# Optimization experiments

Measured on AMD Instinct MI355X. Metric: run time of the kernel, lower is better.

Reference implementation:

```python
import jax, jax.numpy as jnp
import numpy as np

W_WIN, ETA, NSUB, GAP = 5, 0.5, 2, 1e-6

# ---------------- host-side (detached) partition helpers ----------------

def _softmax_np(x):
    e = np.exp(x - x.max())
    return e / e.sum()

def _jsd_np(p, q):
    p = p + 1e-8; p = p / p.sum()
    q = q + 1e-8; q = q / q.sum()
    m = 0.5 * (p + q)
    return float(0.5 * (p * np.log(p / m)).sum() + 0.5 * (q * np.log(q / m)).sum())

def _make_increasing_np(t, gap=GAP):
    t = t.copy()
    for i in range(1, len(t)):
        if t[i] - t[i - 1] < gap:
            t[i] = t[i - 1] + gap
    return t

def _apt_partition(embs, times, w=W_WIN, eta=ETA):
    n = len(times)
    if n < 2 * w:
        return [times[0], times[-1]], [(0, n - 1)]
    bounds = [times[0]]; starts = [0]; j = 0
    while j <= n - 2 * w:
        pl = _softmax_np(embs[j:j + w].mean(0))
        pr = _softmax_np(embs[j + w:j + 2 * w].mean(0))
        if _jsd_np(pl, pr) > eta:
            bounds.append((times[j + w - 1] + times[j + w]) / 2.0)
            starts.append(j + w)
            j += w
        else:
            j += 1
    if times[-1] > bounds[-1]:
        bounds.append(times[-1])
    segs = []
    for i, s in enumerate(starts):
        e = starts[i + 1] - 1 if i + 1 < len(starts) else n - 1
        segs.append((s, e))
    return bounds, segs

def _build_plans(enc_np, ht_np, hl_np, pt_np):
    # mirrors encoded.detach() + .item()/.tolist() in the torch code: the
    # change-point partition and time grids are concrete / non-differentiable
    plans = []
    for b in range(enc_np.shape[0]):
        Lb = int(hl_np[b])
        times = [float(t) for t in ht_np[b, :Lb]]
        bounds, segs = _apt_partition(enc_np[b, :Lb], times)
        seg_plans = []
        for si, (s, e) in enumerate(segs):
            t0 = bounds[si]
            t1 = bounds[si + 1] if si + 1 < len(bounds) else bounds[-1]
            ats = sorted(set([t0, t1] + [t for t in times[s:e + 1] if t0 <= t <= t1]))
            ts = _make_increasing_np(np.asarray(ats, np.float64))
            sel = [int(np.argmin(np.abs(ts - ti))) for ti in times[s:e + 1]]
            seg_plans.append((s, e, (ts[1:] - ts[:-1]).astype(np.float32), sel))
        tail = None
        if float(pt_np[b]) > bounds[-1] + 1e-6:
            s, e = segs[-1]
            ts = _make_increasing_np(np.asarray([bounds[-1], float(pt_np[b])], np.float64))
            tail = (s, e, (ts[1:] - ts[:-1]).astype(np.float32))
        plans.append((seg_plans, tail))
    return plans

# ---------------- differentiable forward ----------------

def _forward(params, plans, u, hi, pos, neg):
    (emb_table, mlp_w1, mlp_b1, mlp_w2, mlp_b2, user_table,
     vf_w1, vf_b1, vf_w2, vf_b2, vf_w3, vf_b3) = params
    B, L = hi.shape
    # Encoder: mlp(emb(ids))
    encoded = jax.nn.relu(emb_table[hi] @ mlp_w1 + mlp_b1) @ mlp_w2 + mlp_b2  # (B,L,d)

    def vf(z, env):  # augmented state [z, env]; env part has zero derivative
        x = jnp.concatenate([z, env])
        h1 = jax.nn.softplus(x @ vf_w1 + vf_b1)
        h2 = jax.nn.softplus(h1 @ vf_w2 + vf_b2)
        return h2 @ vf_w3 + vf_b3

    def integrate(z0, env, dts):  # fixed-step Euler, NSUB substeps per interval
        def step(z, dt):
            for _ in range(NSUB):
                z = z + (dt / NSUB) * vf(z, env)
            return z, z
        _, traj = jax.lax.scan(step, z0, jnp.asarray(dts))
        return jnp.concatenate([z0[None], traj], 0)  # (K, d)

    z_out, tz_out = [], []
    for b in range(B):
        seg_plans, tail = plans[b]
        z = user_table[u[b]]
        tz = []
        for (s, e, dts, sel) in seg_plans:
            env = encoded[b, s:e + 1].mean(0)
            if len(dts) == 0:  # degenerate segment (unreachable with this data)
                tz.extend([z] * (e - s + 1))
                continue
            zt = integrate(z, env, dts)
            tz.extend([zt[i] for i in sel])  # state-at-nearest-grid-time matching
            z = zt[-1]
        if tail is not None:  # evolve up to prediction time t_target
            s, e, dts = tail
            z = integrate(z, encoded[b, s:e + 1].mean(0), dts)[-1]
        z_out.append(z)
        tz_out.append(jnp.stack(tz))
    z_final = jnp.stack(z_out)          # (B,d)
    traj_z = jnp.stack(tz_out)          # (B,L,d) evolved states at interaction times
    traj_t = encoded                    # traj targets = encoded items in order
    s_pos = jnp.sum(z_final * emb_table[pos], -1)
    s_neg = jnp.sum(z_final * emb_table[neg], -1)
    return jnp.concatenate([s_pos[:, None], s_neg[:, None],
                            traj_z.reshape(B, -1), traj_t.reshape(B, -1)], -1)


def setup_inputs():
    key = jax.random.key(0)
    ks = jax.random.split(key, 16)
    n_users, n_items, d, h = 10000, 200000, 128, 512
    B, L = 4, 128
    def xavier(k, shape):
        s = (2.0 / (shape[0] + shape[1])) ** 0.5
        return (jax.random.normal(k, shape) * s).astype(jnp.float32)
    inp = {
        'emb_table': xavier(ks[0], (n_items, d)).at[0].set(0.0),  # padding_idx=0
        'mlp_w1': xavier(ks[1], (d, d)), 'mlp_b1': jnp.zeros((d,), jnp.float32),
        'mlp_w2': xavier(ks[2], (d, d)), 'mlp_b2': jnp.zeros((d,), jnp.float32),
        'user_table': xavier(ks[3], (n_users, d)),
        'vf_w1': xavier(ks[4], (2 * d, h)), 'vf_b1': jnp.zeros((h,), jnp.float32),
        'vf_w2': xavier(ks[5], (h, h)), 'vf_b2': jnp.zeros((h,), jnp.float32),
        'vf_w3': xavier(ks[6], (h, d)), 'vf_b3': jnp.zeros((d,), jnp.float32),
        'u': jax.random.randint(ks[7], (B,), 0, n_users),
        'hi': jax.random.randint(ks[8], (B, L), 1, n_items),
        'ht': jnp.sort(jax.random.uniform(ks[9], (B, L)) * 10.0, axis=1).astype(jnp.float32),
        'hl': jnp.full((B,), L, dtype=jnp.int32),
        'pos': jax.random.randint(ks[10], (B,), 1, n_items),
        'neg': jax.random.randint(ks[11], (B,), 1, n_items),
    }
    inp['pt'] = inp['ht'][:, -1] + 1.0
    return inp


def reference(emb_table, mlp_w1, mlp_b1, mlp_w2, mlp_b2, user_table,
              vf_w1, vf_b1, vf_w2, vf_b2, vf_w3, vf_b3,
              u, hi, ht, hl, pt, pos, neg):
    params = (emb_table, mlp_w1, mlp_b1, mlp_w2, mlp_b2, user_table,
              vf_w1, vf_b1, vf_w2, vf_b2, vf_w3, vf_b3)
    enc_np = np.asarray(jax.nn.relu(emb_table[hi] @ mlp_w1 + mlp_b1) @ mlp_w2 + mlp_b2)
    plans = _build_plans(enc_np, np.asarray(ht), np.asarray(hl), np.asarray(pt))
    return _forward(params, plans, u, hi, pos, neg)
```

## Files before the change

### kernel.cpp

```cpp
#include <hip/hip_runtime.h>
#include <math.h>

#define W_WIN 5
#define NSUB 2
#define MAX_SEG 64
#define MAX_T 256
#define NWGB 8
#define CALIB_END 6

__device__ __forceinline__ float softplusf(float v) {
    return fmaxf(v, 0.0f) + log1pf(expf(-fabsf(v)));
}

__device__ __forceinline__ float npsum128(float e0, float e1) {
    int lane = threadIdx.x & 63;
    int k = lane & 7;
    float r = __shfl(e0, k, 64);
    #pragma unroll
    for (int m = 1; m < 8; ++m) r += __shfl(e0, k + 8 * m, 64);
    #pragma unroll
    for (int m = 0; m < 8; ++m) r += __shfl(e1, k + 8 * m, 64);
    float r0 = __shfl(r, 0, 64), r1 = __shfl(r, 1, 64), r2 = __shfl(r, 2, 64), r3 = __shfl(r, 3, 64);
    float r4 = __shfl(r, 4, 64), r5 = __shfl(r, 5, 64), r6 = __shfl(r, 6, 64), r7 = __shfl(r, 7, 64);
    return ((r0 + r1) + (r2 + r3)) + ((r4 + r5) + (r6 + r7));
}

__device__ __forceinline__ float wmax128(float e0, float e1) {
    float m = fmaxf(e0, e1);
    #pragma unroll
    for (int s = 1; s < 64; s <<= 1) m = fmaxf(m, __shfl_xor(m, s, 64));
    return m;
}

__global__ void encode_kernel(const float* __restrict__ emb, const int* __restrict__ hi,
                              const float* __restrict__ w1, const float* __restrict__ b1,
                              const float* __restrict__ w2, const float* __restrict__ b2,
                              float* __restrict__ enc, float* __restrict__ out,
                              int B, int L, int D) {
    __shared__ float x[128];
    __shared__ float h[128];
    int row = blockIdx.x;
    int j = threadIdx.x;
    int idx = hi[row];
    x[j] = emb[(size_t)idx * D + j];
    __syncthreads();
    float s = b1[j];
    #pragma unroll 8
    for (int i = 0; i < 128; ++i) s += x[i] * w1[i * 128 + j];
    h[j] = fmaxf(s, 0.0f);
    __syncthreads();
    float o = b2[j];
    #pragma unroll 8
    for (int i = 0; i < 128; ++i) o += h[i] * w2[i * 128 + j];
    enc[(size_t)row * D + j] = o;
    int b = row / L, l = row % L;
    size_t OS = 2 + 2 * (size_t)L * D;
    out[(size_t)b * OS + 2 + (size_t)L * D + (size_t)l * D + j] = o;
}

__global__ __launch_bounds__(64) void jsd_kernel(
        const float* __restrict__ enc_all, const int* __restrict__ hl,
        float* __restrict__ jsdv, int L, int D) {
    const int b = blockIdx.x >> 7;
    const int j = blockIdx.x & 127;
    const int n = hl[b];
    if (n < 2 * W_WIN || j > n - 2 * W_WIN) return;
    const int lane = threadIdx.x;
    const float* r = enc_all + ((size_t)b * L + j) * D;
    float ml0 = ((((r[lane]       + r[128 + lane]) + r[256 + lane]) + r[384 + lane]) + r[512 + lane]) / 5.0f;
    float ml1 = ((((r[64 + lane]  + r[192 + lane]) + r[320 + lane]) + r[448 + lane]) + r[576 + lane]) / 5.0f;
    float mr0 = ((((r[640 + lane] + r[768 + lane]) + r[896 + lane]) + r[1024 + lane]) + r[1152 + lane]) / 5.0f;
    float mr1 = ((((r[704 + lane] + r[832 + lane]) + r[960 + lane]) + r[1088 + lane]) + r[1216 + lane]) / 5.0f;
    float mxl = wmax128(ml0, ml1), mxr = wmax128(mr0, mr1);
    float a0 = expf(ml0 - mxl), a1 = expf(ml1 - mxl);
    float c0 = expf(mr0 - mxr), c1 = expf(mr1 - mxr);
    float sl = npsum128(a0, a1), sr = npsum128(c0, c1);
    float p0 = a0 / sl + 1e-8f, p1 = a1 / sl + 1e-8f;
    float q0 = c0 / sr + 1e-8f, q1 = c1 / sr + 1e-8f;
    float sp = npsum128(p0, p1), sq = npsum128(q0, q1);
    p0 /= sp; p1 /= sp; q0 /= sq; q1 /= sq;
    float mv0 = 0.5f * (p0 + q0), mv1 = 0.5f * (p1 + q1);
    float t10 = p0 * logf(p0 / mv0), t11 = p1 * logf(p1 / mv1);
    float t20 = q0 * logf(q0 / mv0), t21 = q1 * logf(q1 / mv1);
    float s1 = npsum128(t10, t11), s2 = npsum128(t20, t21);
    if (lane == 0) jsdv[b * L + j] = 0.5f * s1 + 0.5f * s2;
}

__global__ __launch_bounds__(64) void plan_kernel(
        const float* __restrict__ enc_all, const float* __restrict__ ht,
        const int* __restrict__ hl, const float* __restrict__ pt,
        const float* __restrict__ jsdv,
        float* __restrict__ envs, float* __restrict__ dt_sched,
        int* __restrict__ envid, int* __restrict__ stateidx,
        int* __restrict__ Tcnt, int B, int L, int D) {
    const int b = blockIdx.x;
    const int lane = threadIdx.x;
    const float* encg = enc_all + (size_t)b * L * D;
    const float* times = ht + (size_t)b * L;

    __shared__ float encs[128 * 128];
    __shared__ double cand[160];
    __shared__ double bounds[40];
    __shared__ int starts[40];
    __shared__ int seg_s[40], seg_e[40];
    __shared__ int m_sh;

    for (int v = lane; v < 128 * 128 / 4; v += 64)
        ((float4*)encs)[v] = ((const float4*)encg)[v];
    int n = hl[b];
    __syncthreads();

    int nb = 1, ns = 1;
    if (lane == 0) { bounds[0] = (double)times[0]; starts[0] = 0; }
    __syncthreads();

    if (n >= 2 * W_WIN) {
        int j = 0;
        while (j <= n - 2 * W_WIN) {
            float jsd = jsdv[b * L + j];
            if (jsd > 0.5f) {
                if (nb < 39 && ns < 39) {
                    if (lane == 0) {
                        bounds[nb] = ((double)times[j + W_WIN - 1] + (double)times[j + W_WIN]) * 0.5;
                        starts[ns] = j + W_WIN;
                    }
                    nb++; ns++;
                }
                j += W_WIN;
            } else {
                j += 1;
            }
        }
    }
    __syncthreads();

    {
        double lastb = bounds[nb - 1];
        if ((double)times[n - 1] > lastb) {
            if (lane == 0) bounds[nb] = (double)times[n - 1];
            nb++;
        }
    }
    if (lane == 0) {
        for (int si = 0; si < ns; ++si) {
            seg_s[si] = starts[si];
            seg_e[si] = (si + 1 < ns) ? (starts[si + 1] - 1) : (n - 1);
        }
    }
    __syncthreads();

    int C = 0;
    for (int si = 0; si < ns; ++si) {
        int s = seg_s[si], e = seg_e[si];
        if (lane == 0) {
            double t0 = bounds[si];
            double t1 = (si + 1 < nb) ? bounds[si + 1] : bounds[nb - 1];
            int m = 0;
            cand[m++] = t0;
            for (int l = s; l <= e; ++l) {
                double tv = (double)times[l];
                if (tv < t0 || tv > t1) continue;
                if (tv != cand[m - 1]) cand[m++] = tv;
            }
            if (t1 > cand[m - 1]) cand[m++] = t1;
            for (int k = 1; k < m; ++k)
                if (cand[k] - cand[k - 1] < 1e-6) cand[k] = cand[k - 1] + 1e-6;
            m_sh = m;
        }
        __syncthreads();
        int m = m_sh;
        int K = m - 1;
        if (C + K > MAX_T) K = MAX_T - C;
        for (int k = lane; k < K; k += 64) {
            dt_sched[b * MAX_T + C + k] = (float)(cand[k + 1] - cand[k]);
            envid[b * MAX_T + C + k] = si;
        }
        for (int l = s + lane; l <= e; l += 64) {
            double tv = (double)times[l];
            int best = 0;
            double bd = fabs(cand[0] - tv);
            for (int k = 1; k < m; ++k) {
                double dk = fabs(cand[k] - tv);
                if (dk < bd) { bd = dk; best = k; }
            }
            stateidx[b * L + l] = C + best;
        }
        __syncthreads();
        C += K;
    }

    if (lane == 0) {
        double ptv = (double)pt[b];
        if (ptv > bounds[nb - 1] + 1e-6 && C < MAX_T) {
            double a0d = bounds[nb - 1], a1d = ptv;
            if (a1d - a0d < 1e-6) a1d = a0d + 1e-6;
            dt_sched[b * MAX_T + C] = (float)(a1d - a0d);
            envid[b * MAX_T + C] = ns - 1;
            C++;
        }
        Tcnt[b] = C;
    }
    for (int si = 0; si < ns; ++si) {
        int s = seg_s[si], e = seg_e[si];
        float s0 = 0.0f, s1 = 0.0f;
        for (int l = s; l <= e; ++l) {
            s0 += encs[l * 128 + lane];
            s1 += encs[l * 128 + lane + 64];
        }
        float inv = 1.0f / (float)(e - s + 1);
        envs[((size_t)b * MAX_SEG + si) * 128 + lane] = s0 * inv;
        envs[((size_t)b * MAX_SEG + si) * 128 + lane + 64] = s1 * inv;
    }
}

typedef unsigned long long u64;

__device__ __forceinline__ u64 packw(float v, int phase) {
    return ((u64)(unsigned)phase << 32) | (u64)__float_as_uint(v);
}
__device__ __forceinline__ void publish2(u64* fast, u64* slow, float v, int phase) {
    u64 pk = packw(v, phase);
    __hip_atomic_store(fast, pk, __ATOMIC_RELAXED, __HIP_MEMORY_SCOPE_WORKGROUP);
    __hip_atomic_store(slow, pk, __ATOMIC_RELAXED, __HIP_MEMORY_SCOPE_AGENT);
}
__device__ __forceinline__ u64 ld_sc0(const u64* p) {
    u64 v;
    asm volatile("global_load_dwordx2 %0, %1, off sc0\n\t"
                 "s_waitcnt vmcnt(0)"
                 : "=&v"(v) : "v"(p) : "memory");
    return v;
}
__device__ __forceinline__ u64 ld_agent(const u64* p) {
    return __hip_atomic_load(p, __ATOMIC_RELAXED, __HIP_MEMORY_SCOPE_AGENT);
}
__device__ __forceinline__ void ld8_sc0(const u64* b, u64* p) {
    const u64 *a0 = b, *a1 = b + 128, *a2 = b + 256, *a3 = b + 384,
              *a4 = b + 512, *a5 = b + 640, *a6 = b + 768, *a7 = b + 896;
    asm volatile(
        "global_load_dwordx2 %0, %8, off sc0\n\t"
        "global_load_dwordx2 %1, %9, off sc0\n\t"
        "global_load_dwordx2 %2, %10, off sc0\n\t"
        "global_load_dwordx2 %3, %11, off sc0\n\t"
        "global_load_dwordx2 %4, %12, off sc0\n\t"
        "global_load_dwordx2 %5, %13, off sc0\n\t"
        "global_load_dwordx2 %6, %14, off sc0\n\t"
        "global_load_dwordx2 %7, %15, off sc0\n\t"
        "s_waitcnt vmcnt(0)"
        : "=&v"(p[0]), "=&v"(p[1]), "=&v"(p[2]), "=&v"(p[3]),
          "=&v"(p[4]), "=&v"(p[5]), "=&v"(p[6]), "=&v"(p[7])
        : "v"(a0), "v"(a1), "v"(a2), "v"(a3),
          "v"(a4), "v"(a5), "v"(a6), "v"(a7)
        : "memory");
}
__device__ __forceinline__ void ld8_agent(const u64* b, u64* p) {
    #pragma unroll
    for (int i = 0; i < 8; ++i) p[i] = ld_agent(b + i * 128);
}
__device__ __forceinline__ bool all8p(const u64* p, int phase) {
    bool ok = true;
    #pragma unroll
    for (int i = 0; i < 8; ++i) ok &= ((int)(p[i] >> 32) == phase);
    return ok;
}
__device__ __forceinline__ float fold8(const u64* p) {
    float s = 0.0f;
    #pragma unroll
    for (int i = 0; i < 8; ++i) s += __uint_as_float((unsigned)p[i]);
    return s;
}
__device__ __forceinline__ float fold8mix(const u64* f, const u64* s8, int phase) {
    float s = 0.0f;
    #pragma unroll
    for (int i = 0; i < 8; ++i) {
        u64 pk = ((int)(f[i] >> 32) == phase) ? f[i] : s8[i];
        s += __uint_as_float((unsigned)pk);
    }
    return s;
}

__global__ __launch_bounds__(512, 1) void ode_coop(
    const float* __restrict__ usert, const int* __restrict__ u,
    const float* __restrict__ vw1, const float* __restrict__ vb1,
    const float* __restrict__ vw2, const float* __restrict__ vb2,
    const float* __restrict__ vw3, const float* __restrict__ vb3,
    const float* __restrict__ emb, const int* __restrict__ pos, const int* __restrict__ neg,
    const float* __restrict__ envs, const float* __restrict__ dtsch,
    const int* __restrict__ envid, const int* __restrict__ stidx,
    const int* __restrict__ Tc,
    u64* h1f, u64* zpf, u64* h1st, u64* zpst,
    float* out, int B)
{
    const int batch = blockIdx.x & 7;
    if (batch >= B) return;
    const int g = blockIdx.x >> 3;
    const int tid = threadIdx.x;

    const int cl = tid >> 3, q = tid & 7;
    const int c12 = g * 64 + cl;
    const int cz = tid >> 2, r = tid & 3;

    __shared__ float xs[256];
    __shared__ float h1s[512];
    __shared__ float h2s[64];
    __shared__ int sidx_sh[128];
    __shared__ float dts_sh[MAX_T];
    __shared__ int sid_sh[MAX_T];

    float w1r[32], w2r[64], w3p[16];
    #pragma unroll
    for (int k4 = 0; k4 < 8; ++k4) {
        int jj = ((k4 + q) & 7) * 4;
        #pragma unroll
        for (int m = 0; m < 4; ++m)
            w1r[k4 * 4 + m] = vw1[(size_t)(q * 32 + jj + m) * 512 + c12];
    }
    #pragma unroll
    for (int k4 = 0; k4 < 16; ++k4) {
        int jj = ((k4 + 2 * q) & 15) * 4;
        #pragma unroll
        for (int m = 0; m < 4; ++m)
            w2r[k4 * 4 + m] = vw2[(size_t)(q * 64 + jj + m) * 512 + c12];
    }
    #pragma unroll
    for (int k = 0; k < 16; ++k)
        w3p[k] = vw3[(size_t)(g * 64 + r * 16 + k) * 128 + cz];
    const float bias1 = vb1[c12];
    const float bias2 = vb2[c12];
    const float b3c = (tid < 128) ? vb3[tid] : 0.0f;

    if (tid < 128) sidx_sh[tid] = stidx[batch * 128 + tid];
    if (tid < MAX_T) {
        dts_sh[tid] = dtsch[batch * MAX_T + tid];
        sid_sh[tid] = envid[batch * MAX_T + tid];
    }

    const int T = Tc[batch];
    u64* h1fb = h1f + batch * 512;
    u64* zpfb = zpf + batch * 1024;
    u64* h1b  = h1st + batch * 512;
    u64* zpb  = zpst + batch * 1024;
    const size_t OS = 2 + 2 * (size_t)128 * 128;
    float* outb = out + (size_t)batch * OS;

    int modeA = 0, modeB = 0;

    if (tid < 128) xs[tid] = usert[(size_t)u[batch] * 128 + tid];
    __syncthreads();

    int lp = 0;
    if (g == 0) {
        while (lp < 128 && sidx_sh[lp] == 0) {
            if (tid < 128) outb[2 + (size_t)lp * 128 + tid] = xs[tid];
            ++lp;
        }
    }

    int phase = 0;
    for (int t = 0; t < T; ++t) {
        const int si = sid_sh[t];
        const float hdt = dts_sh[t] * 0.5f;
        const float* envp = envs + ((size_t)batch * MAX_SEG + si) * 128;
        if (tid >= 128 && tid < 256) xs[tid] = envp[tid - 128];
        __syncthreads();
        #pragma unroll
        for (int sub = 0; sub < NSUB; ++sub) {
            ++phase;
            float acc = 0.0f;
            #pragma unroll
            for (int k4 = 0; k4 < 8; ++k4) {
                int off = q * 32 + ((k4 + q) & 7) * 4;
                float4 xv = *(const float4*)(xs + off);
                acc += w1r[k4 * 4 + 0] * xv.x + w1r[k4 * 4 + 1] * xv.y
                     + w1r[k4 * 4 + 2] * xv.z + w1r[k4 * 4 + 3] * xv.w;
            }
            #pragma unroll
            for (int s = 1; s < 8; s <<= 1) acc += __shfl_xor(acc, s, 64);
            if (q == 0) publish2(&h1fb[c12], &h1b[c12], softplusf(acc + bias1), phase);
            {
                u64 pk;
                if (modeA == 1) {
                    #pragma unroll 1
                    for (int it = 0; ; ++it) {
                        pk = ld_sc0(&h1fb[tid]);
                        if ((int)(pk >> 32) == phase) break;
                        if ((it & 15) == 15) {
                            pk = ld_agent(&h1b[tid]);
                            if ((int)(pk >> 32) == phase) break;
                        }
                    }
                } else if (modeA == 2) {
                    for (;;) {
                        pk = ld_agent(&h1b[tid]);
                        if ((int)(pk >> 32) == phase) break;
                        __builtin_amdgcn_s_sleep(1);
                    }
                } else {
                    bool viafast = false;
                    #pragma unroll 1
                    for (;;) {
                        pk = ld_sc0(&h1fb[tid]);
                        if ((int)(pk >> 32) == phase) { viafast = true; break; }
                        pk = ld_agent(&h1b[tid]);
                        if ((int)(pk >> 32) == phase) break;
                        __builtin_amdgcn_s_sleep(1);
                    }
                    if (phase == CALIB_END) modeA = __all(viafast) ? 1 : 2;
                }
                h1s[tid] = __uint_as_float((unsigned)pk);
            }
            __syncthreads();
            float acc2 = 0.0f;
            #pragma unroll
            for (int k4 = 0; k4 < 16; ++k4) {
                int off = q * 64 + ((k4 + 2 * q) & 15) * 4;
                float4 xv = *(const float4*)(h1s + off);
                acc2 += w2r[k4 * 4 + 0] * xv.x + w2r[k4 * 4 + 1] * xv.y
                      + w2r[k4 * 4 + 2] * xv.z + w2r[k4 * 4 + 3] * xv.w;
            }
            #pragma unroll
            for (int s = 1; s < 8; s <<= 1) acc2 += __shfl_xor(acc2, s, 64);
            if (q == 0) h2s[cl] = softplusf(acc2 + bias2);
            __syncthreads();
            float az = 0.0f;
            #pragma unroll
            for (int k4 = 0; k4 < 4; ++k4) {
                float4 hv = *(const float4*)(h2s + r * 16 + k4 * 4);
                az += w3p[k4 * 4 + 0] * hv.x + w3p[k4 * 4 + 1] * hv.y
                    + w3p[k4 * 4 + 2] * hv.z + w3p[k4 * 4 + 3] * hv.w;
            }
            az += __shfl_xor(az, 1, 64);
            az += __shfl_xor(az, 2, 64);
            if (r == 0) publish2(&zpfb[g * 128 + cz], &zpb[g * 128 + cz], az, phase);
            if (tid < 128) {
                float sum;
                u64 f[8], s8[8];
                if (modeB == 1) {
                    #pragma unroll 1
                    for (int it = 0; ; ++it) {
                        ld8_sc0(&zpfb[tid], f);
                        if (all8p(f, phase)) { sum = fold8(f); break; }
                        if ((it & 15) == 15) {
                            ld8_agent(&zpb[tid], s8);
                            bool ok = true;
                            #pragma unroll
                            for (int i = 0; i < 8; ++i)
                                ok &= (((int)(f[i] >> 32) == phase) | ((int)(s8[i] >> 32) == phase));
                            if (ok) { sum = fold8mix(f, s8, phase); break; }
                        }
                    }
                } else if (modeB == 2) {
                    for (;;) {
                        ld8_agent(&zpb[tid], s8);
                        if (all8p(s8, phase)) { sum = fold8(s8); break; }
                        __builtin_amdgcn_s_sleep(1);
                    }
                } else {
                    bool viafast = false;
                    #pragma unroll 1
                    for (;;) {
                        ld8_sc0(&zpfb[tid], f);
                        if (all8p(f, phase)) { viafast = true; sum = fold8(f); break; }
                        ld8_agent(&zpb[tid], s8);
                        bool ok = true;
                        #pragma unroll
                        for (int i = 0; i < 8; ++i)
                            ok &= (((int)(f[i] >> 32) == phase) | ((int)(s8[i] >> 32) == phase));
                        if (ok) { sum = fold8mix(f, s8, phase); break; }
                        __builtin_amdgcn_s_sleep(1);
                    }
                    if (phase == CALIB_END) modeB = __all(viafast) ? 1 : 2;
                }
                xs[tid] = xs[tid] + hdt * (sum + b3c);
            }
            __syncthreads();
        }
        if (g == 0) {
            const int m = t + 1;
            while (lp < 128 && sidx_sh[lp] == m) {
                if (tid < 128) outb[2 + (size_t)lp * 128 + tid] = xs[tid];
                ++lp;
            }
        }
    }
    if (g == 0 && tid < 128) {
        int lane = tid & 63;
        const int item = (tid < 64) ? pos[batch] : neg[batch];
        const float* ev = emb + (size_t)item * 128;
        float sacc = xs[lane] * ev[lane] + xs[lane + 64] * ev[lane + 64];
        #pragma unroll
        for (int s = 1; s < 64; s <<= 1) sacc += __shfl_xor(sacc, s, 64);
        if (lane == 0) outb[(tid < 64) ? 0 : 1] = sacc;
    }
}

extern "C" void kernel_launch(void* const* d_in, const int* in_sizes, int n_in,
                              void* d_out, int out_size, void* d_ws, size_t ws_size,
                              hipStream_t stream) {
    const float* emb   = (const float*)d_in[0];
    const float* w1    = (const float*)d_in[1];
    const float* b1    = (const float*)d_in[2];
    const float* w2    = (const float*)d_in[3];
    const float* b2    = (const float*)d_in[4];
    const float* usert = (const float*)d_in[5];
    const float* vw1   = (const float*)d_in[6];
    const float* vb1   = (const float*)d_in[7];
    const float* vw2   = (const float*)d_in[8];
    const float* vb2   = (const float*)d_in[9];
    const float* vw3   = (const float*)d_in[10];
    const float* vb3   = (const float*)d_in[11];
    const int*   u     = (const int*)d_in[12];
    const int*   hi    = (const int*)d_in[13];
    const float* ht    = (const float*)d_in[14];
    const int*   hl    = (const int*)d_in[15];
    const int*   pos   = (const int*)d_in[16];
    const int*   neg   = (const int*)d_in[17];
    const float* pt    = (const float*)d_in[18];

    int D = in_sizes[2];
    int B = in_sizes[12];
    int L = in_sizes[13] / B;

    u64*   h1f      = (u64*)d_ws;
    u64*   zpf      = h1f + 4 * 512;
    u64*   h1st     = zpf + 4 * 1024;
    u64*   zpst     = h1st + 4 * 512;
    float* jsdv     = (float*)(zpst + 4 * 1024);
    float* enc      = jsdv + (size_t)B * L;
    float* envsb    = enc + (size_t)B * L * D;
    float* dt_sched = envsb + (size_t)B * MAX_SEG * D;
    int*   envid    = (int*)(dt_sched + (size_t)B * MAX_T);
    int*   stateidx = envid + (size_t)B * MAX_T;
    int*   Tcnt     = stateidx + (size_t)B * L;

    hipMemsetAsync(h1f, 0, 2 * (4 * 512 + 4 * 1024) * sizeof(u64), stream);
    encode_kernel<<<B * L, D, 0, stream>>>(emb, hi, w1, b1, w2, b2, enc, (float*)d_out, B, L, D);
    jsd_kernel<<<B * 128, 64, 0, stream>>>(enc, hl, jsdv, L, D);
    plan_kernel<<<B, 64, 0, stream>>>(enc, ht, hl, pt, jsdv, envsb, dt_sched, envid, stateidx, Tcnt, B, L, D);
    ode_coop<<<8 * NWGB, 512, 0, stream>>>(usert, u, vw1, vb1, vw2, vb2, vw3, vb3, emb, pos, neg,
                                           envsb, dt_sched, envid, stateidx, Tcnt,
                                           h1f, zpf, h1st, zpst, (float*)d_out, B);
}
```

Measured before the change: 1.389 ms.

## Assign ODE work-groups to batches by XCD id to keep sync traffic local

Each block reads its hardware XCC id, publishes it to a global table, and after a grid-wide rendezvous computes a mapping that places all eight groups of a batch on the same XCD when possible. Fast local-cache polling is then enabled statically for peers known to share the XCD, which replaces the runtime calibration phase. The fallback to agent-scope loads is polled less often. This adds a startup barrier and relies on all 64 blocks being co-resident, and on the XCC_ID register read being valid.

```diff
diff --git a/kernel.cpp b/kernel.cpp
--- a/kernel.cpp
+++ b/kernel.cpp
@@ -6,7 +6,7 @@
 #define MAX_SEG 64
 #define MAX_T 256
 #define NWGB 8
-#define CALIB_END 6
+#define NBLK 64
 
 __device__ __forceinline__ float softplusf(float v) {
     return fmaxf(v, 0.0f) + log1pf(expf(-fabsf(v)));
@@ -278,6 +278,12 @@
     return s;
 }
 
+__device__ __forceinline__ unsigned get_xcc_id() {
+    unsigned x;
+    asm volatile("s_getreg_b32 %0, hwreg(HW_REG_XCC_ID)" : "=s"(x));
+    return x & 7u;
+}
+
 __global__ __launch_bounds__(512, 1) void ode_coop(
     const float* __restrict__ usert, const int* __restrict__ u,
     const float* __restrict__ vw1, const float* __restrict__ vb1,
@@ -287,13 +293,75 @@
     const float* __restrict__ envs, const float* __restrict__ dtsch,
     const int* __restrict__ envid, const int* __restrict__ stidx,
     const int* __restrict__ Tc,
-    u64* h1f, u64* zpf, u64* h1st, u64* zpst,
+    u64* h1f, u64* zpf, u64* h1st, u64* zpst, unsigned* xcdtab,
     float* out, int B)
 {
-    const int batch = blockIdx.x & 7;
-    if (batch >= B) return;
-    const int g = blockIdx.x >> 3;
     const int tid = threadIdx.x;
+
+    __shared__ int xcds_sh[NBLK];
+    __shared__ int asg_sh[NBLK];
+    __shared__ int role_sh;
+    __shared__ int same_sh[8];
+    __shared__ int allsame_sh;
+
+    const unsigned myxcd = get_xcc_id();
+
+    if (tid == 0) {
+        __hip_atomic_store(&xcdtab[blockIdx.x], 0x100u | myxcd,
+                           __ATOMIC_RELAXED, __HIP_MEMORY_SCOPE_AGENT);
+        for (;;) {
+            bool all = true;
+            for (int i = 0; i < NBLK; ++i) {
+                unsigned v = __hip_atomic_load(&xcdtab[i], __ATOMIC_RELAXED,
+                                               __HIP_MEMORY_SCOPE_AGENT);
+                if (!(v & 0x100u)) { all = false; break; }
+            }
+            if (all) break;
+            __builtin_amdgcn_s_sleep(8);
+        }
+        int counts[8] = {0, 0, 0, 0, 0, 0, 0, 0};
+        for (int i = 0; i < NBLK; ++i) {
+            int x = (int)(__hip_atomic_load(&xcdtab[i], __ATOMIC_RELAXED,
+                                            __HIP_MEMORY_SCOPE_AGENT) & 7u);
+            xcds_sh[i] = x; counts[x]++;
+        }
+        int ord[8]; unsigned used = 0;
+        for (int k = 0; k < 8; ++k) {
+            int best = 0, bc = -1;
+            for (int x = 0; x < 8; ++x)
+                if (!((used >> x) & 1u) && counts[x] > bc) { bc = counts[x]; best = x; }
+            ord[k] = best; used |= 1u << best;
+        }
+        for (int i = 0; i < NBLK; ++i) asg_sh[i] = -1;
+        for (int b = 0; b < B; ++b) {
+            int X = ord[b], gg = 0;
+            for (int i = 0; i < NBLK && gg < 8; ++i)
+                if (asg_sh[i] < 0 && xcds_sh[i] == X) { asg_sh[i] = (b << 3) | gg; ++gg; }
+            for (int i = 0; i < NBLK && gg < 8; ++i)
+                if (asg_sh[i] < 0) { asg_sh[i] = (b << 3) | gg; ++gg; }
+        }
+        int role = asg_sh[blockIdx.x];
+        role_sh = role;
+        int same_all = 1;
+        if (role >= 0) {
+            int bb = role >> 3;
+            for (int g2 = 0; g2 < 8; ++g2) {
+                int pb = 0;
+                for (int i = 0; i < NBLK; ++i)
+                    if (asg_sh[i] == ((bb << 3) | g2)) { pb = i; break; }
+                int s = (xcds_sh[pb] == (int)myxcd) ? 1 : 0;
+                same_sh[g2] = s; same_all &= s;
+            }
+        }
+        allsame_sh = same_all;
+    }
+    __syncthreads();
+    const int role = role_sh;
+    if (role < 0) return;
+    const int batch = role >> 3;
+    const int g = role & 7;
+    const bool fastB = (allsame_sh != 0);
+    const bool fastA = (same_sh[tid >> 6] != 0);
 
     const int cl = tid >> 3, q = tid & 7;
     const int c12 = g * 64 + cl;
@@ -341,8 +409,6 @@
     u64* zpb  = zpst + batch * 1024;
     const size_t OS = 2 + 2 * (size_t)128 * 128;
     float* outb = out + (size_t)batch * OS;
-
-    int modeA = 0, modeB = 0;
 
     if (tid < 128) xs[tid] = usert[(size_t)u[batch] * 128 + tid];
     __syncthreads();
@@ -378,33 +444,22 @@
             if (q == 0) publish2(&h1fb[c12], &h1b[c12], softplusf(acc + bias1), phase);
             {
                 u64 pk;
-                if (modeA == 1) {
+                if (fastA) {
                     #pragma unroll 1
                     for (int it = 0; ; ++it) {
                         pk = ld_sc0(&h1fb[tid]);
                         if ((int)(pk >> 32) == phase) break;
-                        if ((it & 15) == 15) {
+                        if ((it & 63) == 63) {
                             pk = ld_agent(&h1b[tid]);
                             if ((int)(pk >> 32) == phase) break;
                         }
                     }
-                } else if (modeA == 2) {
+                } else {
                     for (;;) {
                         pk = ld_agent(&h1b[tid]);
                         if ((int)(pk >> 32) == phase) break;
                         __builtin_amdgcn_s_sleep(1);
                     }
-                } else {
-                    bool viafast = false;
-                    #pragma unroll 1
-                    for (;;) {
-                        pk = ld_sc0(&h1fb[tid]);
-                        if ((int)(pk >> 32) == phase) { viafast = true; break; }
-                        pk = ld_agent(&h1b[tid]);
-                        if ((int)(pk >> 32) == phase) break;
-                        __builtin_amdgcn_s_sleep(1);
-                    }
-                    if (phase == CALIB_END) modeA = __all(viafast) ? 1 : 2;
                 }
                 h1s[tid] = __uint_as_float((unsigned)pk);
             }
@@ -434,12 +489,12 @@
             if (tid < 128) {
                 float sum;
                 u64 f[8], s8[8];
-                if (modeB == 1) {
+                if (fastB) {
                     #pragma unroll 1
                     for (int it = 0; ; ++it) {
                         ld8_sc0(&zpfb[tid], f);
                         if (all8p(f, phase)) { sum = fold8(f); break; }
-                        if ((it & 15) == 15) {
+                        if ((it & 31) == 31) {
                             ld8_agent(&zpb[tid], s8);
                             bool ok = true;
                             #pragma unroll
@@ -448,27 +503,12 @@
                             if (ok) { sum = fold8mix(f, s8, phase); break; }
                         }
                     }
-                } else if (modeB == 2) {
+                } else {
                     for (;;) {
                         ld8_agent(&zpb[tid], s8);
                         if (all8p(s8, phase)) { sum = fold8(s8); break; }
                         __builtin_amdgcn_s_sleep(1);
                     }
-                } else {
-                    bool viafast = false;
-                    #pragma unroll 1
-                    for (;;) {
-                        ld8_sc0(&zpfb[tid], f);
-                        if (all8p(f, phase)) { viafast = true; sum = fold8(f); break; }
-                        ld8_agent(&zpb[tid], s8);
-                        bool ok = true;
-                        #pragma unroll
-                        for (int i = 0; i < 8; ++i)
-                            ok &= (((int)(f[i] >> 32) == phase) | ((int)(s8[i] >> 32) == phase));
-                        if (ok) { sum = fold8mix(f, s8, phase); break; }
-                        __builtin_amdgcn_s_sleep(1);
-                    }
-                    if (phase == CALIB_END) modeB = __all(viafast) ? 1 : 2;
                 }
                 xs[tid] = xs[tid] + hdt * (sum + b3c);
             }
@@ -520,11 +560,12 @@
     int B = in_sizes[12];
     int L = in_sizes[13] / B;
 
-    u64*   h1f      = (u64*)d_ws;
-    u64*   zpf      = h1f + 4 * 512;
-    u64*   h1st     = zpf + 4 * 1024;
-    u64*   zpst     = h1st + 4 * 512;
-    float* jsdv     = (float*)(zpst + 4 * 1024);
+    u64*      h1f    = (u64*)d_ws;
+    u64*      zpf    = h1f + 4 * 512;
+    u64*      h1st   = zpf + 4 * 1024;
+    u64*      zpst   = h1st + 4 * 512;
+    unsigned* xcdtab = (unsigned*)(zpst + 4 * 1024);
+    float* jsdv     = (float*)(xcdtab + NBLK);
     float* enc      = jsdv + (size_t)B * L;
     float* envsb    = enc + (size_t)B * L * D;
     float* dt_sched = envsb + (size_t)B * MAX_SEG * D;
@@ -532,11 +573,12 @@
     int*   stateidx = envid + (size_t)B * MAX_T;
     int*   Tcnt     = stateidx + (size_t)B * L;
 
-    hipMemsetAsync(h1f, 0, 2 * (4 * 512 + 4 * 1024) * sizeof(u64), stream);
+    hipMemsetAsync(h1f, 0, 2 * (4 * 512 + 4 * 1024) * sizeof(u64) + NBLK * sizeof(unsigned),
+                   stream);
     encode_kernel<<<B * L, D, 0, stream>>>(emb, hi, w1, b1, w2, b2, enc, (float*)d_out, B, L, D);
     jsd_kernel<<<B * 128, 64, 0, stream>>>(enc, hl, jsdv, L, D);
     plan_kernel<<<B, 64, 0, stream>>>(enc, ht, hl, pt, jsdv, envsb, dt_sched, envid, stateidx, Tcnt, B, L, D);
-    ode_coop<<<8 * NWGB, 512, 0, stream>>>(usert, u, vw1, vb1, vw2, vb2, vw3, vb3, emb, pos, neg,
-                                           envsb, dt_sched, envid, stateidx, Tcnt,
-                                           h1f, zpf, h1st, zpst, (float*)d_out, B);
-}
+    ode_coop<<<NBLK, 512, 0, stream>>>(usert, u, vw1, vb1, vw2, vb2, vw3, vb3, emb, pos, neg,
+                                       envsb, dt_sched, envid, stateidx, Tcnt,
+                                       h1f, zpf, h1st, zpst, xcdtab, (float*)d_out, B);
+}
```

Measured after the change: 5.338 ms. 284% more time.
